# Kernel optimization log

Measured on AMD Instinct MI355X. Metric: run time of the kernel, lower is better.

Reference implementation:

```python
import jax, jax.numpy as jnp
import numpy as np

B, S, F_IN, E, H = 8, 1024, 512, 512, 8
C = E // H  # chunk size per head


def setup_inputs() -> dict:
    key = jax.random.key(0)
    ks = jax.random.split(key, 20)
    sF = 1.0 / np.sqrt(F_IN)
    sE = 1.0 / np.sqrt(E)
    d = {
        'x_real': jax.random.normal(ks[0], (B, S, F_IN), jnp.float32),
        'x_imag': jax.random.normal(ks[1], (B, S, F_IN), jnp.float32),
    }
    names = ['q', 'k', 'v']
    for i, n in enumerate(names):
        d[f'w{n}_r'] = jax.random.normal(ks[2 + 4 * i], (E, F_IN), jnp.float32) * sF
        d[f'w{n}_i'] = jax.random.normal(ks[3 + 4 * i], (E, F_IN), jnp.float32) * sF
        d[f'b{n}_r'] = jax.random.normal(ks[4 + 4 * i], (E,), jnp.float32) * sF
        d[f'b{n}_i'] = jax.random.normal(ks[5 + 4 * i], (E,), jnp.float32) * sF
    d['wo_r'] = jax.random.normal(ks[14], (F_IN, E), jnp.float32) * sE
    d['wo_i'] = jax.random.normal(ks[15], (F_IN, E), jnp.float32) * sE
    d['bo_r'] = jax.random.normal(ks[16], (F_IN,), jnp.float32) * sE
    d['bo_i'] = jax.random.normal(ks[17], (F_IN,), jnp.float32) * sE
    return d


def _cplx(r, i):
    return jax.lax.complex(r, i)


def _heads(y):
    # (B, S, E) -> (B, H, S, C); matches split(dim=2)+stack+transpose(0,1)
    return y.reshape(B, S, H, C).transpose(0, 2, 1, 3)


def reference(x_real, x_imag,
              wq_r, wq_i, bq_r, bq_i,
              wk_r, wk_i, bk_r, bk_i,
              wv_r, wv_i, bv_r, bv_i,
              wo_r, wo_i, bo_r, bo_i):
    x = _cplx(x_real, x_imag)
    wq, wk, wv = _cplx(wq_r, wq_i), _cplx(wk_r, wk_i), _cplx(wv_r, wv_i)
    bq, bk, bv = _cplx(bq_r, bq_i), _cplx(bk_r, bk_i), _cplx(bv_r, bv_i)
    wo, bo = _cplx(wo_r, wo_i), _cplx(bo_r, bo_i)

    q = _heads(jnp.einsum('bsf,ef->bse', x, wq) + bq)  # (B,H,S,C) complex
    k = _heads(jnp.einsum('bsf,ef->bse', x, wk) + bk)
    v = _heads(jnp.einsum('bsf,ef->bse', x, wv) + bv)

    divisor = jnp.sqrt(jnp.float32(2 * C))
    # Hermitian inner product: q @ conj(k)^T -> (B,H,S,S)
    sim = jnp.einsum('bhsc,bhtc->bhst', q, jnp.conj(k)) / divisor
    attn = jax.nn.softmax(jnp.abs(sim), axis=3).astype(jnp.complex64)
    # second Hermitian bmm: attn @ conj(v)
    av = jnp.einsum('bhst,bhtc->bhsc', attn, jnp.conj(v))
    concat = av.transpose(0, 2, 1, 3).reshape(B, S, E)
    out = jnp.einsum('bse,fe->bsf', concat, wo) + bo
    return out, attn
```

## Files before the change

### kernel.cpp

```cpp
#include <hip/hip_runtime.h>


namespace {
constexpr int Bn = 8, Sn = 1024, Fn = 512, En = 512, Hn = 8, Cn = 64;
constexpr int Mn = Bn * Sn;
constexpr int Qszi = Bn * Hn * Sn * Cn;
constexpr size_t Qsz = (size_t)Qszi;
constexpr int XLIM = Bn * Sn * Fn;
constexpr int WLIM = En * Fn;
constexpr size_t OUT1 = (size_t)Bn * Sn * Fn;
constexpr size_t ATT1 = (size_t)Bn * Hn * Sn * Sn;
constexpr float RDIV = 0.08838834764831845f;
}

typedef __attribute__((ext_vector_type(8))) short short8v;
typedef __attribute__((ext_vector_type(4))) float f32x4;

__device__ __forceinline__ float bf2f(unsigned short u) {
    union { unsigned int u32; float f; } c; c.u32 = (unsigned int)u << 16; return c.f;
}
__device__ __forceinline__ unsigned short f2bf(float f) {
    union { float f; unsigned int u; } c; c.f = f;
    unsigned int r = (c.u + 0x7FFFu + ((c.u >> 16) & 1u)) >> 16;
    return (unsigned short)r;
}
__device__ __forceinline__ unsigned int packbf(float lo, float hi) {
    return (unsigned int)f2bf(lo) | ((unsigned int)f2bf(hi) << 16);
}
__device__ __forceinline__ short8v neg8(short8v v) {
    union { short8v s; unsigned int u[4]; } c; c.s = v;
    #pragma unroll
    for (int j = 0; j < 4; ++j) c.u[j] ^= 0x80008000u;
    return c.s;
}
__device__ __forceinline__ float4 ld4(const float* p) { return *(const float4*)p; }

template<bool CONJB>
__device__ __forceinline__ void mfma_body(
    const short (*As_r)[40], const short (*As_i)[40],
    const short (*Bs_r)[40], const short (*Bs_i)[40],
    int wr, int wn, int lrow, int lk,
    f32x4 accr[4][2], f32x4 acci[4][2])
{
    short8v a_r[4], a_i[4], a_x[4];
    #pragma unroll
    for (int fm = 0; fm < 4; ++fm) {
        a_r[fm] = *(const short8v*)&As_r[wr*64 + fm*16 + lrow][lk];
        a_i[fm] = *(const short8v*)&As_i[wr*64 + fm*16 + lrow][lk];
        a_x[fm] = neg8(CONJB ? a_r[fm] : a_i[fm]);
    }
    short8v b_r[2], b_i[2];
    #pragma unroll
    for (int fn = 0; fn < 2; ++fn) {
        b_r[fn] = *(const short8v*)&Bs_r[wn*32 + fn*16 + lrow][lk];
        b_i[fn] = *(const short8v*)&Bs_i[wn*32 + fn*16 + lrow][lk];
    }
    #pragma unroll
    for (int fm = 0; fm < 4; ++fm)
        #pragma unroll
        for (int fn = 0; fn < 2; ++fn) {
            accr[fm][fn] = __builtin_amdgcn_mfma_f32_16x16x32_bf16(
                a_r[fm], b_r[fn], accr[fm][fn], 0, 0, 0);
            accr[fm][fn] = __builtin_amdgcn_mfma_f32_16x16x32_bf16(
                CONJB ? a_i[fm] : a_x[fm], b_i[fn], accr[fm][fn], 0, 0, 0);
            acci[fm][fn] = __builtin_amdgcn_mfma_f32_16x16x32_bf16(
                CONJB ? a_x[fm] : a_r[fm], b_i[fn], acci[fm][fn], 0, 0, 0);
            acci[fm][fn] = __builtin_amdgcn_mfma_f32_16x16x32_bf16(
                a_i[fm], b_r[fn], acci[fm][fn], 0, 0, 0);
        }
}

template<bool CONJB>
__device__ __forceinline__ void cgemm_mfma(
    const float* __restrict__ Ar, const float* __restrict__ Ai, int arow0, int lda,
    const float* __restrict__ Br, const float* __restrict__ Bi, int brow0, int ldb,
    int K, f32x4 accr[4][2], f32x4 acci[4][2])
{
    __shared__ short As_r[128][40], As_i[128][40];
    __shared__ short Bs_r[64][40],  Bs_i[64][40];
    const int tid = threadIdx.x;
    const int sar = tid >> 1, sac = (tid & 1) * 16;
    const int sbr = tid >> 2, sbc = (tid & 3) * 8;
    const int wid = tid >> 6, lane = tid & 63;
    const int wr = wid >> 1, wn = wid & 1;
    const int lrow = lane & 15, lk = (lane >> 4) * 8;

    for (int k0 = 0; k0 < K; k0 += 32) {
        const float* pAr = Ar + (size_t)(arow0 + sar) * lda + k0 + sac;
        const float* pAi = Ai + (size_t)(arow0 + sar) * lda + k0 + sac;
        float4 va_r[4], va_i[4];
        #pragma unroll
        for (int q = 0; q < 4; ++q) { va_r[q] = ld4(pAr + 4*q); va_i[q] = ld4(pAi + 4*q); }
        const float* pBr = Br + (size_t)(brow0 + sbr) * ldb + k0 + sbc;
        const float* pBi = Bi + (size_t)(brow0 + sbr) * ldb + k0 + sbc;
        float4 vb_r[2], vb_i[2];
        #pragma unroll
        for (int q = 0; q < 2; ++q) { vb_r[q] = ld4(pBr + 4*q); vb_i[q] = ld4(pBi + 4*q); }

        __syncthreads();
        #pragma unroll
        for (int q = 0; q < 4; ++q) {
            *(uint2*)&As_r[sar][sac + 4*q] =
                make_uint2(packbf(va_r[q].x, va_r[q].y), packbf(va_r[q].z, va_r[q].w));
            *(uint2*)&As_i[sar][sac + 4*q] =
                make_uint2(packbf(va_i[q].x, va_i[q].y), packbf(va_i[q].z, va_i[q].w));
        }
        #pragma unroll
        for (int q = 0; q < 2; ++q) {
            *(uint2*)&Bs_r[sbr][sbc + 4*q] =
                make_uint2(packbf(vb_r[q].x, vb_r[q].y), packbf(vb_r[q].z, vb_r[q].w));
            *(uint2*)&Bs_i[sbr][sbc + 4*q] =
                make_uint2(packbf(vb_i[q].x, vb_i[q].y), packbf(vb_i[q].z, vb_i[q].w));
        }
        __syncthreads();
        mfma_body<CONJB>(As_r, As_i, Bs_r, Bs_i, wr, wn, lrow, lk, accr, acci);
    }
}

template<bool CONJB>
__device__ __forceinline__ void cgemm_mfma_abf16(
    const unsigned short* __restrict__ Ar, const unsigned short* __restrict__ Ai,
    int arow0, int lda,
    const float* __restrict__ Br, const float* __restrict__ Bi, int brow0, int ldb,
    int K, f32x4 accr[4][2], f32x4 acci[4][2])
{
    __shared__ short As_r[128][40], As_i[128][40];
    __shared__ short Bs_r[64][40],  Bs_i[64][40];
    const int tid = threadIdx.x;
    const int sar = tid >> 1, sac = (tid & 1) * 16;
    const int sbr = tid >> 2, sbc = (tid & 3) * 8;
    const int wid = tid >> 6, lane = tid & 63;
    const int wr = wid >> 1, wn = wid & 1;
    const int lrow = lane & 15, lk = (lane >> 4) * 8;

    for (int k0 = 0; k0 < K; k0 += 32) {
        const unsigned short* pAr = Ar + (size_t)(arow0 + sar) * lda + k0 + sac;
        const unsigned short* pAi = Ai + (size_t)(arow0 + sar) * lda + k0 + sac;
        short8v va_r0 = *(const short8v*)pAr;
        short8v va_r1 = *(const short8v*)(pAr + 8);
        short8v va_i0 = *(const short8v*)pAi;
        short8v va_i1 = *(const short8v*)(pAi + 8);
        const float* pBr = Br + (size_t)(brow0 + sbr) * ldb + k0 + sbc;
        const float* pBi = Bi + (size_t)(brow0 + sbr) * ldb + k0 + sbc;
        float4 vb_r[2], vb_i[2];
        #pragma unroll
        for (int q = 0; q < 2; ++q) { vb_r[q] = ld4(pBr + 4*q); vb_i[q] = ld4(pBi + 4*q); }

        __syncthreads();
        *(short8v*)&As_r[sar][sac]     = va_r0;
        *(short8v*)&As_r[sar][sac + 8] = va_r1;
        *(short8v*)&As_i[sar][sac]     = va_i0;
        *(short8v*)&As_i[sar][sac + 8] = va_i1;
        #pragma unroll
        for (int q = 0; q < 2; ++q) {
            *(uint2*)&Bs_r[sbr][sbc + 4*q] =
                make_uint2(packbf(vb_r[q].x, vb_r[q].y), packbf(vb_r[q].z, vb_r[q].w));
            *(uint2*)&Bs_i[sbr][sbc + 4*q] =
                make_uint2(packbf(vb_i[q].x, vb_i[q].y), packbf(vb_i[q].z, vb_i[q].w));
        }
        __syncthreads();
        mfma_body<CONJB>(As_r, As_i, Bs_r, Bs_i, wr, wn, lrow, lk, accr, acci);
    }
}

__global__ void diag_k(float* __restrict__ out, float v) { out[0] = v; }

__global__ __launch_bounds__(256) void qkv_proj_k(
    const float* __restrict__ xr, const float* __restrict__ xi,
    const float* __restrict__ wqr, const float* __restrict__ wqi,
    const float* __restrict__ bqr, const float* __restrict__ bqi,
    const float* __restrict__ wkr, const float* __restrict__ wki,
    const float* __restrict__ bkr, const float* __restrict__ bki,
    const float* __restrict__ wvr, const float* __restrict__ wvi,
    const float* __restrict__ bvr, const float* __restrict__ bvi,
    unsigned short* __restrict__ ws)
{
    const int which = blockIdx.z;
    const float* wr_ = which == 0 ? wqr : which == 1 ? wkr : wvr;
    const float* wi_ = which == 0 ? wqi : which == 1 ? wki : wvi;
    const float* br_ = which == 0 ? bqr : which == 1 ? bkr : bvr;
    const float* bi_ = which == 0 ? bqi : which == 1 ? bki : bvi;
    unsigned short* outr = ws + (size_t)which * 2 * Qsz;
    unsigned short* outi = outr + Qsz;

    const int m0 = blockIdx.x * 128, n0 = blockIdx.y * 64;
    f32x4 accr[4][2], acci[4][2];
    const f32x4 z4 = {0.f, 0.f, 0.f, 0.f};
    #pragma unroll
    for (int fm = 0; fm < 4; ++fm)
        #pragma unroll
        for (int fn = 0; fn < 2; ++fn) { accr[fm][fn] = z4; acci[fm][fn] = z4; }

    cgemm_mfma<false>(xr, xi, m0, Fn, wr_, wi_, n0, Fn, Fn, accr, acci);

    const int lane = threadIdx.x & 63, wid = threadIdx.x >> 6;
    const int wr2 = wid >> 1, wn2 = wid & 1;
    #pragma unroll
    for (int fm = 0; fm < 4; ++fm)
        #pragma unroll
        for (int fn = 0; fn < 2; ++fn) {
            const int e = n0 + wn2*32 + fn*16 + (lane & 15);
            const int h = e >> 6, c = e & (Cn - 1);
            const float brv = br_[e], biv = bi_[e];
            #pragma unroll
            for (int r = 0; r < 4; ++r) {
                const int m = m0 + wr2*64 + fm*16 + (lane >> 4)*4 + r;
                const int b = m >> 10, s = m & (Sn - 1);
                const size_t idx = (((size_t)(b * Hn + h)) * Sn + s) * Cn + c;
                outr[idx] = f2bf(accr[fm][fn][r] + brv);
                outi[idx] = f2bf(acci[fm][fn][r] + biv);
            }
        }
}

template<int ST>
__global__ __launch_bounds__(256) void attn_fused_k(
    const unsigned short* __restrict__ qkv, float* __restrict__ attn,
    unsigned short* __restrict__ avb)
{
    const int bh = blockIdx.y;
    const int r0 = blockIdx.x * 128;
    const size_t poff = (size_t)bh * Sn * Cn;
    const unsigned short* qr = qkv + poff;
    const unsigned short* qi = qkv + Qsz + poff;
    const unsigned short* kr = qkv + 2 * Qsz + poff;
    const unsigned short* ki = qkv + 3 * Qsz + poff;
    const unsigned short* vr = qkv + 4 * Qsz + poff;
    const unsigned short* vi = qkv + 5 * Qsz + poff;

    __shared__ short Qr[128][68], Qi[128][68];
    __shared__ short KP[2][64][68];
    __shared__ short Vtr[64][68], Vti[64][68];
    short (*Ps)[68] = (short(*)[68])KP;

    const int tid = threadIdx.x;
    const int lane = tid & 63, wid = tid >> 6;
    const int lrow = lane & 15, g = lane >> 4, lk = g * 8;
    const int srow0 = 32 * wid;
    const int wr = wid >> 1, wn = wid & 1;

    {
        const int row = tid >> 1, seg = (tid & 1) * 32;
        const unsigned short* pr = qr + (size_t)(r0 + row) * Cn + seg;
        const unsigned short* pi = qi + (size_t)(r0 + row) * Cn + seg;
        #pragma unroll
        for (int q = 0; q < 4; ++q) {
            *(short8v*)&Qr[row][seg + 8*q] = *(const short8v*)(pr + 8*q);
            *(short8v*)&Qi[row][seg + 8*q] = *(const short8v*)(pi + 8*q);
        }
    }
    const int kst_row = tid >> 2, kst_seg = (tid & 3) * 16;
    const int vst_t = tid & 63, vst_c = (tid >> 6) * 16;

    float ssum[2][4] = {};
    __syncthreads();

    for (int t0 = 0; t0 < Sn; t0 += 64) {
        short8v k_r0 = *(const short8v*)(kr + (size_t)(t0 + kst_row) * Cn + kst_seg);
        short8v k_r1 = *(const short8v*)(kr + (size_t)(t0 + kst_row) * Cn + kst_seg + 8);
        short8v k_i0 = *(const short8v*)(ki + (size_t)(t0 + kst_row) * Cn + kst_seg);
        short8v k_i1 = *(const short8v*)(ki + (size_t)(t0 + kst_row) * Cn + kst_seg + 8);
        __syncthreads();
        *(short8v*)&KP[0][kst_row][kst_seg]     = k_r0;
        *(short8v*)&KP[0][kst_row][kst_seg + 8] = k_r1;
        *(short8v*)&KP[1][kst_row][kst_seg]     = k_i0;
        *(short8v*)&KP[1][kst_row][kst_seg + 8] = k_i1;
        __syncthreads();

        f32x4 cr[2][4], ci[2][4];
        const f32x4 z4 = {0.f, 0.f, 0.f, 0.f};
        #pragma unroll
        for (int fm = 0; fm < 2; ++fm)
            #pragma unroll
            for (int fn = 0; fn < 4; ++fn) { cr[fm][fn] = z4; ci[fm][fn] = z4; }
        #pragma unroll
        for (int kh = 0; kh < 2; ++kh) {
            const int kof = kh*32 + lk;
            short8v br_[4], bi_[4];
            #pragma unroll
            for (int fn = 0; fn < 4; ++fn) {
                br_[fn] = *(const short8v*)&KP[0][fn*16 + lrow][kof];
                bi_[fn] = *(const short8v*)&KP[1][fn*16 + lrow][kof];
            }
            #pragma unroll
            for (int fm = 0; fm < 2; ++fm) {
                short8v ar = *(const short8v*)&Qr[srow0 + fm*16 + lrow][kof];
                short8v ai = *(const short8v*)&Qi[srow0 + fm*16 + lrow][kof];
                short8v ax = neg8(ar);
                #pragma unroll
                for (int fn = 0; fn < 4; ++fn) {
                    cr[fm][fn] = __builtin_amdgcn_mfma_f32_16x16x32_bf16(ar, br_[fn], cr[fm][fn], 0,0,0);
                    cr[fm][fn] = __builtin_amdgcn_mfma_f32_16x16x32_bf16(ai, bi_[fn], cr[fm][fn], 0,0,0);
                    ci[fm][fn] = __builtin_amdgcn_mfma_f32_16x16x32_bf16(ai, br_[fn], ci[fm][fn], 0,0,0);
                    ci[fm][fn] = __builtin_amdgcn_mfma_f32_16x16x32_bf16(ax, bi_[fn], ci[fm][fn], 0,0,0);
                }
            }
        }
        #pragma unroll
        for (int fm = 0; fm < 2; ++fm)
            #pragma unroll
            for (int rr = 0; rr < 4; ++rr) {
                float acc = 0.f;
                #pragma unroll
                for (int fn = 0; fn < 4; ++fn) {
                    const float re = cr[fm][fn][rr], im = ci[fm][fn][rr];
                    acc += __expf(sqrtf(fmaf(re, re, im*im)) * RDIV);
                }
                ssum[fm][rr] += acc;
            }
    }
    float inv[2][4];
    #pragma unroll
    for (int fm = 0; fm < 2; ++fm)
        #pragma unroll
        for (int rr = 0; rr < 4; ++rr) {
            float s = ssum[fm][rr];
            s += __shfl_xor(s, 1); s += __shfl_xor(s, 2);
            s += __shfl_xor(s, 4); s += __shfl_xor(s, 8);
            inv[fm][rr] = 1.f / s;
        }

    f32x4 pvr[4][2], pvi[4][2];
    const f32x4 z4 = {0.f, 0.f, 0.f, 0.f};
    #pragma unroll
    for (int fm = 0; fm < 4; ++fm)
        #pragma unroll
        for (int fn = 0; fn < 2; ++fn) { pvr[fm][fn] = z4; pvi[fm][fn] = z4; }

    for (int t0 = 0; t0 < Sn; t0 += 64) {
        short8v k_r0 = *(const short8v*)(kr + (size_t)(t0 + kst_row) * Cn + kst_seg);
        short8v k_r1 = *(const short8v*)(kr + (size_t)(t0 + kst_row) * Cn + kst_seg + 8);
        short8v k_i0 = *(const short8v*)(ki + (size_t)(t0 + kst_row) * Cn + kst_seg);
        short8v k_i1 = *(const short8v*)(ki + (size_t)(t0 + kst_row) * Cn + kst_seg + 8);
        short8v v_r0 = *(const short8v*)(vr + (size_t)(t0 + vst_t) * Cn + vst_c);
        short8v v_r1 = *(const short8v*)(vr + (size_t)(t0 + vst_t) * Cn + vst_c + 8);
        short8v v_i0 = *(const short8v*)(vi + (size_t)(t0 + vst_t) * Cn + vst_c);
        short8v v_i1 = *(const short8v*)(vi + (size_t)(t0 + vst_t) * Cn + vst_c + 8);
        __syncthreads();
        *(short8v*)&KP[0][kst_row][kst_seg]     = k_r0;
        *(short8v*)&KP[0][kst_row][kst_seg + 8] = k_r1;
        *(short8v*)&KP[1][kst_row][kst_seg]     = k_i0;
        *(short8v*)&KP[1][kst_row][kst_seg + 8] = k_i1;
        #pragma unroll
        for (int j = 0; j < 8; ++j) {
            Vtr[vst_c + j][vst_t] = v_r0[j];
            Vtr[vst_c + 8 + j][vst_t] = v_r1[j];
            Vti[vst_c + j][vst_t] = v_i0[j];
            Vti[vst_c + 8 + j][vst_t] = v_i1[j];
        }
        __syncthreads();

        f32x4 cr[2][4], ci[2][4];
        #pragma unroll
        for (int fm = 0; fm < 2; ++fm)
            #pragma unroll
            for (int fn = 0; fn < 4; ++fn) { cr[fm][fn] = z4; ci[fm][fn] = z4; }
        #pragma unroll
        for (int kh = 0; kh < 2; ++kh) {
            const int kof = kh*32 + lk;
            short8v br_[4], bi_[4];
            #pragma unroll
            for (int fn = 0; fn < 4; ++fn) {
                br_[fn] = *(const short8v*)&KP[0][fn*16 + lrow][kof];
                bi_[fn] = *(const short8v*)&KP[1][fn*16 + lrow][kof];
            }
            #pragma unroll
            for (int fm = 0; fm < 2; ++fm) {
                short8v ar = *(const short8v*)&Qr[srow0 + fm*16 + lrow][kof];
                short8v ai = *(const short8v*)&Qi[srow0 + fm*16 + lrow][kof];
                short8v ax = neg8(ar);
                #pragma unroll
                for (int fn = 0; fn < 4; ++fn) {
                    cr[fm][fn] = __builtin_amdgcn_mfma_f32_16x16x32_bf16(ar, br_[fn], cr[fm][fn], 0,0,0);
                    cr[fm][fn] = __builtin_amdgcn_mfma_f32_16x16x32_bf16(ai, bi_[fn], cr[fm][fn], 0,0,0);
                    ci[fm][fn] = __builtin_amdgcn_mfma_f32_16x16x32_bf16(ai, br_[fn], ci[fm][fn], 0,0,0);
                    ci[fm][fn] = __builtin_amdgcn_mfma_f32_16x16x32_bf16(ax, bi_[fn], ci[fm][fn], 0,0,0);
                }
            }
        }
        float pval[2][4][4];
        #pragma unroll
        for (int fm = 0; fm < 2; ++fm)
            #pragma unroll
            for (int fn = 0; fn < 4; ++fn) {
                const int t = t0 + fn*16 + lrow;
                #pragma unroll
                for (int rr = 0; rr < 4; ++rr) {
                    const float re = cr[fm][fn][rr], im = ci[fm][fn][rr];
                    const float p = __expf(sqrtf(fmaf(re, re, im*im)) * RDIV) * inv[fm][rr];
                    pval[fm][fn][rr] = p;
                    const size_t row = (size_t)bh * Sn + r0 + srow0 + fm*16 + g*4 + rr;
                    const size_t idx = (row * Sn + t) * (size_t)ST;
                    if (ST == 2) *(float2*)&attn[idx] = make_float2(p, 0.f);
                    else         attn[idx] = p;
                }
            }
        __syncthreads();
        #pragma unroll
        for (int fm = 0; fm < 2; ++fm)
            #pragma unroll
            for (int fn = 0; fn < 4; ++fn)
                #pragma unroll
                for (int rr = 0; rr < 4; ++rr)
                    Ps[srow0 + fm*16 + g*4 + rr][fn*16 + lrow] = f2bf(pval[fm][fn][rr]);
        __syncthreads();

        #pragma unroll
        for (int kh = 0; kh < 2; ++kh) {
            const int kof = kh*32 + lk;
            short8v bR[2], bI[2];
            #pragma unroll
            for (int fn = 0; fn < 2; ++fn) {
                bR[fn] = *(const short8v*)&Vtr[wn*32 + fn*16 + lrow][kof];
                bI[fn] = *(const short8v*)&Vti[wn*32 + fn*16 + lrow][kof];
            }
            #pragma unroll
            for (int fm = 0; fm < 4; ++fm) {
                short8v pA = *(const short8v*)&Ps[wr*64 + fm*16 + lrow][kof];
                #pragma unroll
                for (int fn = 0; fn < 2; ++fn) {
                    pvr[fm][fn] = __builtin_amdgcn_mfma_f32_16x16x32_bf16(pA, bR[fn], pvr[fm][fn], 0,0,0);
                    pvi[fm][fn] = __builtin_amdgcn_mfma_f32_16x16x32_bf16(pA, bI[fn], pvi[fm][fn], 0,0,0);
                }
            }
        }
    }

    const int b = bh >> 3, h = bh & 7;
    #pragma unroll
    for (int fm = 0; fm < 4; ++fm)
        #pragma unroll
        for (int fn = 0; fn < 2; ++fn) {
            const int c = wn*32 + fn*16 + lrow;
            #pragma unroll
            for (int rr = 0; rr < 4; ++rr) {
                const int row = r0 + wr*64 + fm*16 + g*4 + rr;
                const size_t addr = ((size_t)(b * Sn + row)) * En + h * Cn + c;
                avb[addr]       = f2bf( pvr[fm][fn][rr]);
                avb[Qsz + addr] = f2bf(-pvi[fm][fn][rr]);
            }
        }
}

template<int ST>
__global__ __launch_bounds__(256) void out_proj_k(
    const unsigned short* __restrict__ avr, const unsigned short* __restrict__ avi,
    const float* __restrict__ wor, const float* __restrict__ woi,
    const float* __restrict__ bor, const float* __restrict__ boi,
    float* __restrict__ out)
{
    const int m0 = blockIdx.x * 128, n0 = blockIdx.y * 64;
    f32x4 accr[4][2], acci[4][2];
    const f32x4 z4 = {0.f, 0.f, 0.f, 0.f};
    #pragma unroll
    for (int fm = 0; fm < 4; ++fm)
        #pragma unroll
        for (int fn = 0; fn < 2; ++fn) { accr[fm][fn] = z4; acci[fm][fn] = z4; }

    cgemm_mfma_abf16<false>(avr, avi, m0, En, wor, woi, n0, En, En, accr, acci);

    const int lane = threadIdx.x & 63, wid = threadIdx.x >> 6;
    const int wr2 = wid >> 1, wn2 = wid & 1;
    #pragma unroll
    for (int fm = 0; fm < 4; ++fm)
        #pragma unroll
        for (int fn = 0; fn < 2; ++fn) {
            const int f = n0 + wn2*32 + fn*16 + (lane & 15);
            const float brv = bor[f], biv = boi[f];
            #pragma unroll
            for (int r = 0; r < 4; ++r) {
                const int m = m0 + wr2*64 + fm*16 + (lane >> 4)*4 + r;
                const size_t idx = ((size_t)m * Fn + f) * (size_t)ST;
                if (ST == 2)
                    *(float2*)&out[idx] = make_float2(accr[fm][fn][r] + brv, acci[fm][fn][r] + biv);
                else
                    out[idx] = accr[fm][fn][r] + brv;
            }
        }
}

template<int ST>
static void launch_all(const float* xr, const float* xi,
                       const float* wqr, const float* wqi, const float* bqr, const float* bqi,
                       const float* wkr, const float* wki, const float* bkr, const float* bki,
                       const float* wvr, const float* wvi, const float* bvr, const float* bvi,
                       const float* wor, const float* woi, const float* bor, const float* boi,
                       unsigned short* qkv, unsigned short* avb, float* out, hipStream_t stream)
{
    float* attn = out + OUT1 * ST;
    qkv_proj_k<<<dim3(Mn/128, En/64, 3), 256, 0, stream>>>(
        xr, xi, wqr, wqi, bqr, bqi, wkr, wki, bkr, bki, wvr, wvi, bvr, bvi, qkv);
    attn_fused_k<ST><<<dim3(Sn/128, Bn*Hn), 256, 0, stream>>>(qkv, attn, avb);
    out_proj_k<ST><<<dim3(Mn/128, Fn/64), 256, 0, stream>>>(
        avb, avb + Qsz, wor, woi, bor, boi, out);
}

extern "C" void kernel_launch(void* const* d_in, const int* in_sizes, int n_in,
                              void* d_out, int out_size, void* d_ws, size_t ws_size,
                              hipStream_t stream)
{
    bool sizes_ok = (n_in == 18);
    if (sizes_ok) {
        sizes_ok = in_sizes[0] == XLIM && in_sizes[1] == XLIM;
        for (int g = 0; g < 3 && sizes_ok; ++g) {
            sizes_ok = in_sizes[2 + 4*g] == WLIM && in_sizes[3 + 4*g] == WLIM &&
                       in_sizes[4 + 4*g] == En  && in_sizes[5 + 4*g] == En;
        }
        sizes_ok = sizes_ok && in_sizes[14] == WLIM && in_sizes[15] == WLIM &&
                   in_sizes[16] == Fn && in_sizes[17] == Fn;
    }
    const size_t ws_needed = 8 * Qsz * sizeof(unsigned short);
    const bool ws_ok = (d_ws != nullptr) && (ws_size >= ws_needed);

    const long long fullF = 2LL * (long long)(OUT1 + ATT1);
    const long long realF = (long long)(OUT1 + ATT1);
    const int st = ((long long)out_size == fullF) ? 2
                 : ((long long)out_size == realF) ? 1 : 0;

    if (!sizes_ok || !ws_ok || st == 0) {
        float diag = !sizes_ok ? 3.0e9f
                   : !ws_ok    ? (float)(double)ws_size
                               : (float)out_size;
        diag_k<<<1, 1, 0, stream>>>((float*)d_out, diag);
        return;
    }

    const float* xr  = (const float*)d_in[0];
    const float* xi  = (const float*)d_in[1];
    const float* wqr = (const float*)d_in[2];
    const float* wqi = (const float*)d_in[3];
    const float* bqr = (const float*)d_in[4];
    const float* bqi = (const float*)d_in[5];
    const float* wkr = (const float*)d_in[6];
    const float* wki = (const float*)d_in[7];
    const float* bkr = (const float*)d_in[8];
    const float* bki = (const float*)d_in[9];
    const float* wvr = (const float*)d_in[10];
    const float* wvi = (const float*)d_in[11];
    const float* bvr = (const float*)d_in[12];
    const float* bvi = (const float*)d_in[13];
    const float* wor = (const float*)d_in[14];
    const float* woi = (const float*)d_in[15];
    const float* bor = (const float*)d_in[16];
    const float* boi = (const float*)d_in[17];

    unsigned short* qkv = (unsigned short*)d_ws;
    unsigned short* avb = qkv + 6 * Qsz;
    float* out = (float*)d_out;

    if (st == 2)
        launch_all<2>(xr, xi, wqr, wqi, bqr, bqi, wkr, wki, bkr, bki,
                      wvr, wvi, bvr, bvi, wor, woi, bor, boi, qkv, avb, out, stream);
    else
        launch_all<1>(xr, xi, wqr, wqi, bqr, bqi, wkr, wki, bkr, bki,
                      wvr, wvi, bvr, bvi, wor, woi, bor, boi, qkv, avb, out, stream);
}
```

Baseline: 316.8 us.

## Halve attention query tile to 64 rows and add MFMA wave priority hints

The fused attention kernel now handles 64 query rows per block instead of 128, so each wave owns 16 rows and the grid doubles to 1024 blocks. This cuts registers and LDS per block, which should help occupancy and wave count across the CUs. The cost is that each block rereads K and V for its whole sequence twice (once for the softmax sum, once for the output), so K/V traffic per query row doubles. s_setprio hints are also placed around the MFMA clusters in both the attention and projection GEMMs.

```diff
diff --git a/kernel.cpp b/kernel.cpp
--- a/kernel.cpp
+++ b/kernel.cpp
@@ -55,6 +55,7 @@
         b_r[fn] = *(const short8v*)&Bs_r[wn*32 + fn*16 + lrow][lk];
         b_i[fn] = *(const short8v*)&Bs_i[wn*32 + fn*16 + lrow][lk];
     }
+    __builtin_amdgcn_s_setprio(1);
     #pragma unroll
     for (int fm = 0; fm < 4; ++fm)
         #pragma unroll
@@ -68,6 +69,7 @@
             acci[fm][fn] = __builtin_amdgcn_mfma_f32_16x16x32_bf16(
                 a_i[fm], b_r[fn], acci[fm][fn], 0, 0, 0);
         }
+    __builtin_amdgcn_s_setprio(0);
 }
 
 template<bool CONJB>
@@ -219,7 +221,7 @@
     unsigned short* __restrict__ avb)
 {
     const int bh = blockIdx.y;
-    const int r0 = blockIdx.x * 128;
+    const int r0 = blockIdx.x * 64;
     const size_t poff = (size_t)bh * Sn * Cn;
     const unsigned short* qr = qkv + poff;
     const unsigned short* qi = qkv + Qsz + poff;
@@ -228,7 +230,7 @@
     const unsigned short* vr = qkv + 4 * Qsz + poff;
     const unsigned short* vi = qkv + 5 * Qsz + poff;
 
-    __shared__ short Qr[128][68], Qi[128][68];
+    __shared__ short Qr[64][68], Qi[64][68];
     __shared__ short KP[2][64][68];
     __shared__ short Vtr[64][68], Vti[64][68];
     short (*Ps)[68] = (short(*)[68])KP;
@@ -236,15 +238,15 @@
     const int tid = threadIdx.x;
     const int lane = tid & 63, wid = tid >> 6;
     const int lrow = lane & 15, g = lane >> 4, lk = g * 8;
-    const int srow0 = 32 * wid;
+    const int srow0 = 16 * wid;
     const int wr = wid >> 1, wn = wid & 1;
 
     {
-        const int row = tid >> 1, seg = (tid & 1) * 32;
+        const int row = tid >> 2, seg = (tid & 3) * 16;
         const unsigned short* pr = qr + (size_t)(r0 + row) * Cn + seg;
         const unsigned short* pi = qi + (size_t)(r0 + row) * Cn + seg;
         #pragma unroll
-        for (int q = 0; q < 4; ++q) {
+        for (int q = 0; q < 2; ++q) {
             *(short8v*)&Qr[row][seg + 8*q] = *(const short8v*)(pr + 8*q);
             *(short8v*)&Qi[row][seg + 8*q] = *(const short8v*)(pi + 8*q);
         }
@@ -252,7 +254,7 @@
     const int kst_row = tid >> 2, kst_seg = (tid & 3) * 16;
     const int vst_t = tid & 63, vst_c = (tid >> 6) * 16;
 
-    float ssum[2][4] = {};
+    float ssum[4] = {};
     __syncthreads();
 
     for (int t0 = 0; t0 < Sn; t0 += 64) {
@@ -267,63 +269,52 @@
         *(short8v*)&KP[1][kst_row][kst_seg + 8] = k_i1;
         __syncthreads();
 
-        f32x4 cr[2][4], ci[2][4];
+        f32x4 cr[4], ci[4];
         const f32x4 z4 = {0.f, 0.f, 0.f, 0.f};
         #pragma unroll
-        for (int fm = 0; fm < 2; ++fm)
-            #pragma unroll
-            for (int fn = 0; fn < 4; ++fn) { cr[fm][fn] = z4; ci[fm][fn] = z4; }
+        for (int fn = 0; fn < 4; ++fn) { cr[fn] = z4; ci[fn] = z4; }
         #pragma unroll
         for (int kh = 0; kh < 2; ++kh) {
             const int kof = kh*32 + lk;
-            short8v br_[4], bi_[4];
+            short8v ar = *(const short8v*)&Qr[srow0 + lrow][kof];
+            short8v ai = *(const short8v*)&Qi[srow0 + lrow][kof];
+            short8v ax = neg8(ar);
+            __builtin_amdgcn_s_setprio(1);
             #pragma unroll
             for (int fn = 0; fn < 4; ++fn) {
-                br_[fn] = *(const short8v*)&KP[0][fn*16 + lrow][kof];
-                bi_[fn] = *(const short8v*)&KP[1][fn*16 + lrow][kof];
-            }
-            #pragma unroll
-            for (int fm = 0; fm < 2; ++fm) {
-                short8v ar = *(const short8v*)&Qr[srow0 + fm*16 + lrow][kof];
-                short8v ai = *(const short8v*)&Qi[srow0 + fm*16 + lrow][kof];
-                short8v ax = neg8(ar);
-                #pragma unroll
-                for (int fn = 0; fn < 4; ++fn) {
-                    cr[fm][fn] = __builtin_amdgcn_mfma_f32_16x16x32_bf16(ar, br_[fn], cr[fm][fn], 0,0,0);
-                    cr[fm][fn] = __builtin_amdgcn_mfma_f32_16x16x32_bf16(ai, bi_[fn], cr[fm][fn], 0,0,0);
-                    ci[fm][fn] = __builtin_amdgcn_mfma_f32_16x16x32_bf16(ai, br_[fn], ci[fm][fn], 0,0,0);
-                    ci[fm][fn] = __builtin_amdgcn_mfma_f32_16x16x32_bf16(ax, bi_[fn], ci[fm][fn], 0,0,0);
-                }
-            }
-        }
-        #pragma unroll
-        for (int fm = 0; fm < 2; ++fm)
-            #pragma unroll
-            for (int rr = 0; rr < 4; ++rr) {
-                float acc = 0.f;
-                #pragma unroll
-                for (int fn = 0; fn < 4; ++fn) {
-                    const float re = cr[fm][fn][rr], im = ci[fm][fn][rr];
-                    acc += __expf(sqrtf(fmaf(re, re, im*im)) * RDIV);
-                }
-                ssum[fm][rr] += acc;
-            }
-    }
-    float inv[2][4];
+                short8v br_ = *(const short8v*)&KP[0][fn*16 + lrow][kof];
+                short8v bi_ = *(const short8v*)&KP[1][fn*16 + lrow][kof];
+                cr[fn] = __builtin_amdgcn_mfma_f32_16x16x32_bf16(ar, br_, cr[fn], 0,0,0);
+                cr[fn] = __builtin_amdgcn_mfma_f32_16x16x32_bf16(ai, bi_, cr[fn], 0,0,0);
+                ci[fn] = __builtin_amdgcn_mfma_f32_16x16x32_bf16(ai, br_, ci[fn], 0,0,0);
+                ci[fn] = __builtin_amdgcn_mfma_f32_16x16x32_bf16(ax, bi_, ci[fn], 0,0,0);
+            }
+            __builtin_amdgcn_s_setprio(0);
+        }
+        #pragma unroll
+        for (int rr = 0; rr < 4; ++rr) {
+            float acc = 0.f;
+            #pragma unroll
+            for (int fn = 0; fn < 4; ++fn) {
+                const float re = cr[fn][rr], im = ci[fn][rr];
+                acc += __expf(sqrtf(fmaf(re, re, im*im)) * RDIV);
+            }
+            ssum[rr] += acc;
+        }
+    }
+    float inv[4];
+    #pragma unroll
+    for (int rr = 0; rr < 4; ++rr) {
+        float s = ssum[rr];
+        s += __shfl_xor(s, 1); s += __shfl_xor(s, 2);
+        s += __shfl_xor(s, 4); s += __shfl_xor(s, 8);
+        inv[rr] = 1.f / s;
+    }
+
+    f32x4 pvr[2][2], pvi[2][2];
+    const f32x4 z4 = {0.f, 0.f, 0.f, 0.f};
     #pragma unroll
     for (int fm = 0; fm < 2; ++fm)
-        #pragma unroll
-        for (int rr = 0; rr < 4; ++rr) {
-            float s = ssum[fm][rr];
-            s += __shfl_xor(s, 1); s += __shfl_xor(s, 2);
-            s += __shfl_xor(s, 4); s += __shfl_xor(s, 8);
-            inv[fm][rr] = 1.f / s;
-        }
-
-    f32x4 pvr[4][2], pvi[4][2];
-    const f32x4 z4 = {0.f, 0.f, 0.f, 0.f};
-    #pragma unroll
-    for (int fm = 0; fm < 4; ++fm)
         #pragma unroll
         for (int fn = 0; fn < 2; ++fn) { pvr[fm][fn] = z4; pvi[fm][fn] = z4; }
 
@@ -350,59 +341,48 @@
         }
         __syncthreads();
 
-        f32x4 cr[2][4], ci[2][4];
-        #pragma unroll
-        for (int fm = 0; fm < 2; ++fm)
-            #pragma unroll
-            for (int fn = 0; fn < 4; ++fn) { cr[fm][fn] = z4; ci[fm][fn] = z4; }
+        f32x4 cr[4], ci[4];
+        #pragma unroll
+        for (int fn = 0; fn < 4; ++fn) { cr[fn] = z4; ci[fn] = z4; }
         #pragma unroll
         for (int kh = 0; kh < 2; ++kh) {
             const int kof = kh*32 + lk;
-            short8v br_[4], bi_[4];
+            short8v ar = *(const short8v*)&Qr[srow0 + lrow][kof];
+            short8v ai = *(const short8v*)&Qi[srow0 + lrow][kof];
+            short8v ax = neg8(ar);
+            __builtin_amdgcn_s_setprio(1);
             #pragma unroll
             for (int fn = 0; fn < 4; ++fn) {
-                br_[fn] = *(const short8v*)&KP[0][fn*16 + lrow][kof];
-                bi_[fn] = *(const short8v*)&KP[1][fn*16 + lrow][kof];
-            }
-            #pragma unroll
-            for (int fm = 0; fm < 2; ++fm) {
-                short8v ar = *(const short8v*)&Qr[srow0 + fm*16 + lrow][kof];
-                short8v ai = *(const short8v*)&Qi[srow0 + fm*16 + lrow][kof];
-                short8v ax = neg8(ar);
-                #pragma unroll
-                for (int fn = 0; fn < 4; ++fn) {
-                    cr[fm][fn] = __builtin_amdgcn_mfma_f32_16x16x32_bf16(ar, br_[fn], cr[fm][fn], 0,0,0);
-                    cr[fm][fn] = __builtin_amdgcn_mfma_f32_16x16x32_bf16(ai, bi_[fn], cr[fm][fn], 0,0,0);
-                    ci[fm][fn] = __builtin_amdgcn_mfma_f32_16x16x32_bf16(ai, br_[fn], ci[fm][fn], 0,0,0);
-                    ci[fm][fn] = __builtin_amdgcn_mfma_f32_16x16x32_bf16(ax, bi_[fn], ci[fm][fn], 0,0,0);
-                }
-            }
-        }
-        float pval[2][4][4];
-        #pragma unroll
-        for (int fm = 0; fm < 2; ++fm)
-            #pragma unroll
-            for (int fn = 0; fn < 4; ++fn) {
-                const int t = t0 + fn*16 + lrow;
-                #pragma unroll
-                for (int rr = 0; rr < 4; ++rr) {
-                    const float re = cr[fm][fn][rr], im = ci[fm][fn][rr];
-                    const float p = __expf(sqrtf(fmaf(re, re, im*im)) * RDIV) * inv[fm][rr];
-                    pval[fm][fn][rr] = p;
-                    const size_t row = (size_t)bh * Sn + r0 + srow0 + fm*16 + g*4 + rr;
-                    const size_t idx = (row * Sn + t) * (size_t)ST;
-                    if (ST == 2) *(float2*)&attn[idx] = make_float2(p, 0.f);
-                    else         attn[idx] = p;
-                }
-            }
-        __syncthreads();
-        #pragma unroll
-        for (int fm = 0; fm < 2; ++fm)
-            #pragma unroll
-            for (int fn = 0; fn < 4; ++fn)
-                #pragma unroll
-                for (int rr = 0; rr < 4; ++rr)
-                    Ps[srow0 + fm*16 + g*4 + rr][fn*16 + lrow] = f2bf(pval[fm][fn][rr]);
+                short8v br_ = *(const short8v*)&KP[0][fn*16 + lrow][kof];
+                short8v bi_ = *(const short8v*)&KP[1][fn*16 + lrow][kof];
+                cr[fn] = __builtin_amdgcn_mfma_f32_16x16x32_bf16(ar, br_, cr[fn], 0,0,0);
+                cr[fn] = __builtin_amdgcn_mfma_f32_16x16x32_bf16(ai, bi_, cr[fn], 0,0,0);
+                ci[fn] = __builtin_amdgcn_mfma_f32_16x16x32_bf16(ai, br_, ci[fn], 0,0,0);
+                ci[fn] = __builtin_amdgcn_mfma_f32_16x16x32_bf16(ax, bi_, ci[fn], 0,0,0);
+            }
+            __builtin_amdgcn_s_setprio(0);
+        }
+        float pval[4][4];
+        #pragma unroll
+        for (int fn = 0; fn < 4; ++fn) {
+            const int t = t0 + fn*16 + lrow;
+            #pragma unroll
+            for (int rr = 0; rr < 4; ++rr) {
+                const float re = cr[fn][rr], im = ci[fn][rr];
+                const float p = __expf(sqrtf(fmaf(re, re, im*im)) * RDIV) * inv[rr];
+                pval[fn][rr] = p;
+                const size_t row = (size_t)bh * Sn + r0 + srow0 + g*4 + rr;
+                const size_t idx = (row * Sn + t) * (size_t)ST;
+                if (ST == 2) *(float2*)&attn[idx] = make_float2(p, 0.f);
+                else         attn[idx] = p;
+            }
+        }
+        __syncthreads();
+        #pragma unroll
+        for (int fn = 0; fn < 4; ++fn)
+            #pragma unroll
+            for (int rr = 0; rr < 4; ++rr)
+                Ps[srow0 + g*4 + rr][fn*16 + lrow] = f2bf(pval[fn][rr]);
         __syncthreads();
 
         #pragma unroll
@@ -414,27 +394,29 @@
                 bR[fn] = *(const short8v*)&Vtr[wn*32 + fn*16 + lrow][kof];
                 bI[fn] = *(const short8v*)&Vti[wn*32 + fn*16 + lrow][kof];
             }
-            #pragma unroll
-            for (int fm = 0; fm < 4; ++fm) {
-                short8v pA = *(const short8v*)&Ps[wr*64 + fm*16 + lrow][kof];
+            __builtin_amdgcn_s_setprio(1);
+            #pragma unroll
+            for (int fm = 0; fm < 2; ++fm) {
+                short8v pA = *(const short8v*)&Ps[wr*32 + fm*16 + lrow][kof];
                 #pragma unroll
                 for (int fn = 0; fn < 2; ++fn) {
                     pvr[fm][fn] = __builtin_amdgcn_mfma_f32_16x16x32_bf16(pA, bR[fn], pvr[fm][fn], 0,0,0);
                     pvi[fm][fn] = __builtin_amdgcn_mfma_f32_16x16x32_bf16(pA, bI[fn], pvi[fm][fn], 0,0,0);
                 }
             }
+            __builtin_amdgcn_s_setprio(0);
         }
     }
 
     const int b = bh >> 3, h = bh & 7;
     #pragma unroll
-    for (int fm = 0; fm < 4; ++fm)
+    for (int fm = 0; fm < 2; ++fm)
         #pragma unroll
         for (int fn = 0; fn < 2; ++fn) {
             const int c = wn*32 + fn*16 + lrow;
             #pragma unroll
             for (int rr = 0; rr < 4; ++rr) {
-                const int row = r0 + wr*64 + fm*16 + g*4 + rr;
+                const int row = r0 + wr*32 + fm*16 + g*4 + rr;
                 const size_t addr = ((size_t)(b * Sn + row)) * En + h * Cn + c;
                 avb[addr]       = f2bf( pvr[fm][fn][rr]);
                 avb[Qsz + addr] = f2bf(-pvi[fm][fn][rr]);
@@ -490,7 +472,7 @@
     float* attn = out + OUT1 * ST;
     qkv_proj_k<<<dim3(Mn/128, En/64, 3), 256, 0, stream>>>(
         xr, xi, wqr, wqi, bqr, bqi, wkr, wki, bkr, bki, wvr, wvi, bvr, bvi, qkv);
-    attn_fused_k<ST><<<dim3(Sn/128, Bn*Hn), 256, 0, stream>>>(qkv, attn, avb);
+    attn_fused_k<ST><<<dim3(Sn/64, Bn*Hn), 256, 0, stream>>>(qkv, attn, avb);
     out_proj_k<ST><<<dim3(Mn/128, Fn/64), 256, 0, stream>>>(
         avb, avb + Qsz, wor, woi, bor, boi, out);
 }
```

After: 323.6 us. 2.1% more time.

## Keep Q fragments in registers, give P its own LDS buffer, add MFMA priority

Applied to the files above, without the earlier changes.

Each wave now loads its Q fragments straight from global memory into registers instead of staging them through shared memory, which removes the repeated LDS reads of Q on every key tile. P gets a dedicated shared buffer rather than aliasing the K buffer, so it is written directly in the softmax loop and one barrier goes away. The bf16 conversion of P switches to truncation instead of round-to-nearest, and s_setprio brackets are placed around the MFMA blocks. The changes cost extra registers and a little precision in P.

```diff
diff --git a/kernel.cpp b/kernel.cpp
--- a/kernel.cpp
+++ b/kernel.cpp
@@ -24,6 +24,10 @@
     unsigned int r = (c.u + 0x7FFFu + ((c.u >> 16) & 1u)) >> 16;
     return (unsigned short)r;
 }
+__device__ __forceinline__ unsigned short f2bf_t(float f) {
+    union { float f; unsigned int u; } c; c.f = f;
+    return (unsigned short)(c.u >> 16);
+}
 __device__ __forceinline__ unsigned int packbf(float lo, float hi) {
     return (unsigned int)f2bf(lo) | ((unsigned int)f2bf(hi) << 16);
 }
@@ -55,6 +59,7 @@
         b_r[fn] = *(const short8v*)&Bs_r[wn*32 + fn*16 + lrow][lk];
         b_i[fn] = *(const short8v*)&Bs_i[wn*32 + fn*16 + lrow][lk];
     }
+    __builtin_amdgcn_s_setprio(1);
     #pragma unroll
     for (int fm = 0; fm < 4; ++fm)
         #pragma unroll
@@ -68,6 +73,7 @@
             acci[fm][fn] = __builtin_amdgcn_mfma_f32_16x16x32_bf16(
                 a_i[fm], b_r[fn], acci[fm][fn], 0, 0, 0);
         }
+    __builtin_amdgcn_s_setprio(0);
 }
 
 template<bool CONJB>
@@ -228,10 +234,9 @@
     const unsigned short* vr = qkv + 4 * Qsz + poff;
     const unsigned short* vi = qkv + 5 * Qsz + poff;
 
-    __shared__ short Qr[128][68], Qi[128][68];
-    __shared__ short KP[2][64][68];
+    __shared__ short Ksr[64][68], Ksi[64][68];
     __shared__ short Vtr[64][68], Vti[64][68];
-    short (*Ps)[68] = (short(*)[68])KP;
+    __shared__ short Ps[128][68];
 
     const int tid = threadIdx.x;
     const int lane = tid & 63, wid = tid >> 6;
@@ -239,21 +244,20 @@
     const int srow0 = 32 * wid;
     const int wr = wid >> 1, wn = wid & 1;
 
-    {
-        const int row = tid >> 1, seg = (tid & 1) * 32;
-        const unsigned short* pr = qr + (size_t)(r0 + row) * Cn + seg;
-        const unsigned short* pi = qi + (size_t)(r0 + row) * Cn + seg;
-        #pragma unroll
-        for (int q = 0; q < 4; ++q) {
-            *(short8v*)&Qr[row][seg + 8*q] = *(const short8v*)(pr + 8*q);
-            *(short8v*)&Qi[row][seg + 8*q] = *(const short8v*)(pi + 8*q);
-        }
-    }
+    short8v qfr[2][2], qfi[2][2];
+    #pragma unroll
+    for (int fm = 0; fm < 2; ++fm)
+        #pragma unroll
+        for (int kh = 0; kh < 2; ++kh) {
+            const size_t row = (size_t)(r0 + srow0 + fm*16 + lrow);
+            qfr[fm][kh] = *(const short8v*)(qr + row * Cn + kh*32 + lk);
+            qfi[fm][kh] = *(const short8v*)(qi + row * Cn + kh*32 + lk);
+        }
+
     const int kst_row = tid >> 2, kst_seg = (tid & 3) * 16;
     const int vst_t = tid & 63, vst_c = (tid >> 6) * 16;
 
     float ssum[2][4] = {};
-    __syncthreads();
 
     for (int t0 = 0; t0 < Sn; t0 += 64) {
         short8v k_r0 = *(const short8v*)(kr + (size_t)(t0 + kst_row) * Cn + kst_seg);
@@ -261,10 +265,10 @@
         short8v k_i0 = *(const short8v*)(ki + (size_t)(t0 + kst_row) * Cn + kst_seg);
         short8v k_i1 = *(const short8v*)(ki + (size_t)(t0 + kst_row) * Cn + kst_seg + 8);
         __syncthreads();
-        *(short8v*)&KP[0][kst_row][kst_seg]     = k_r0;
-        *(short8v*)&KP[0][kst_row][kst_seg + 8] = k_r1;
-        *(short8v*)&KP[1][kst_row][kst_seg]     = k_i0;
-        *(short8v*)&KP[1][kst_row][kst_seg + 8] = k_i1;
+        *(short8v*)&Ksr[kst_row][kst_seg]     = k_r0;
+        *(short8v*)&Ksr[kst_row][kst_seg + 8] = k_r1;
+        *(short8v*)&Ksi[kst_row][kst_seg]     = k_i0;
+        *(short8v*)&Ksi[kst_row][kst_seg + 8] = k_i1;
         __syncthreads();
 
         f32x4 cr[2][4], ci[2][4];
@@ -279,13 +283,13 @@
             short8v br_[4], bi_[4];
             #pragma unroll
             for (int fn = 0; fn < 4; ++fn) {
-                br_[fn] = *(const short8v*)&KP[0][fn*16 + lrow][kof];
-                bi_[fn] = *(const short8v*)&KP[1][fn*16 + lrow][kof];
-            }
+                br_[fn] = *(const short8v*)&Ksr[fn*16 + lrow][kof];
+                bi_[fn] = *(const short8v*)&Ksi[fn*16 + lrow][kof];
+            }
+            __builtin_amdgcn_s_setprio(1);
             #pragma unroll
             for (int fm = 0; fm < 2; ++fm) {
-                short8v ar = *(const short8v*)&Qr[srow0 + fm*16 + lrow][kof];
-                short8v ai = *(const short8v*)&Qi[srow0 + fm*16 + lrow][kof];
+                short8v ar = qfr[fm][kh], ai = qfi[fm][kh];
                 short8v ax = neg8(ar);
                 #pragma unroll
                 for (int fn = 0; fn < 4; ++fn) {
@@ -295,6 +299,7 @@
                     ci[fm][fn] = __builtin_amdgcn_mfma_f32_16x16x32_bf16(ax, bi_[fn], ci[fm][fn], 0,0,0);
                 }
             }
+            __builtin_amdgcn_s_setprio(0);
         }
         #pragma unroll
         for (int fm = 0; fm < 2; ++fm)
@@ -337,10 +342,10 @@
         short8v v_i0 = *(const short8v*)(vi + (size_t)(t0 + vst_t) * Cn + vst_c);
         short8v v_i1 = *(const short8v*)(vi + (size_t)(t0 + vst_t) * Cn + vst_c + 8);
         __syncthreads();
-        *(short8v*)&KP[0][kst_row][kst_seg]     = k_r0;
-        *(short8v*)&KP[0][kst_row][kst_seg + 8] = k_r1;
-        *(short8v*)&KP[1][kst_row][kst_seg]     = k_i0;
-        *(short8v*)&KP[1][kst_row][kst_seg + 8] = k_i1;
+        *(short8v*)&Ksr[kst_row][kst_seg]     = k_r0;
+        *(short8v*)&Ksr[kst_row][kst_seg + 8] = k_r1;
+        *(short8v*)&Ksi[kst_row][kst_seg]     = k_i0;
+        *(short8v*)&Ksi[kst_row][kst_seg + 8] = k_i1;
         #pragma unroll
         for (int j = 0; j < 8; ++j) {
             Vtr[vst_c + j][vst_t] = v_r0[j];
@@ -361,13 +366,13 @@
             short8v br_[4], bi_[4];
             #pragma unroll
             for (int fn = 0; fn < 4; ++fn) {
-                br_[fn] = *(const short8v*)&KP[0][fn*16 + lrow][kof];
-                bi_[fn] = *(const short8v*)&KP[1][fn*16 + lrow][kof];
-            }
+                br_[fn] = *(const short8v*)&Ksr[fn*16 + lrow][kof];
+                bi_[fn] = *(const short8v*)&Ksi[fn*16 + lrow][kof];
+            }
+            __builtin_amdgcn_s_setprio(1);
             #pragma unroll
             for (int fm = 0; fm < 2; ++fm) {
-                short8v ar = *(const short8v*)&Qr[srow0 + fm*16 + lrow][kof];
-                short8v ai = *(const short8v*)&Qi[srow0 + fm*16 + lrow][kof];
+                short8v ar = qfr[fm][kh], ai = qfi[fm][kh];
                 short8v ax = neg8(ar);
                 #pragma unroll
                 for (int fn = 0; fn < 4; ++fn) {
@@ -377,8 +382,8 @@
                     ci[fm][fn] = __builtin_amdgcn_mfma_f32_16x16x32_bf16(ax, bi_[fn], ci[fm][fn], 0,0,0);
                 }
             }
-        }
-        float pval[2][4][4];
+            __builtin_amdgcn_s_setprio(0);
+        }
         #pragma unroll
         for (int fm = 0; fm < 2; ++fm)
             #pragma unroll
@@ -388,21 +393,13 @@
                 for (int rr = 0; rr < 4; ++rr) {
                     const float re = cr[fm][fn][rr], im = ci[fm][fn][rr];
                     const float p = __expf(sqrtf(fmaf(re, re, im*im)) * RDIV) * inv[fm][rr];
-                    pval[fm][fn][rr] = p;
                     const size_t row = (size_t)bh * Sn + r0 + srow0 + fm*16 + g*4 + rr;
                     const size_t idx = (row * Sn + t) * (size_t)ST;
                     if (ST == 2) *(float2*)&attn[idx] = make_float2(p, 0.f);
                     else         attn[idx] = p;
+                    Ps[srow0 + fm*16 + g*4 + rr][fn*16 + lrow] = f2bf_t(p);
                 }
             }
-        __syncthreads();
-        #pragma unroll
-        for (int fm = 0; fm < 2; ++fm)
-            #pragma unroll
-            for (int fn = 0; fn < 4; ++fn)
-                #pragma unroll
-                for (int rr = 0; rr < 4; ++rr)
-                    Ps[srow0 + fm*16 + g*4 + rr][fn*16 + lrow] = f2bf(pval[fm][fn][rr]);
         __syncthreads();
 
         #pragma unroll
@@ -414,6 +411,7 @@
                 bR[fn] = *(const short8v*)&Vtr[wn*32 + fn*16 + lrow][kof];
                 bI[fn] = *(const short8v*)&Vti[wn*32 + fn*16 + lrow][kof];
             }
+            __builtin_amdgcn_s_setprio(1);
             #pragma unroll
             for (int fm = 0; fm < 4; ++fm) {
                 short8v pA = *(const short8v*)&Ps[wr*64 + fm*16 + lrow][kof];
@@ -423,6 +421,7 @@
                     pvi[fm][fn] = __builtin_amdgcn_mfma_f32_16x16x32_bf16(pA, bI[fn], pvi[fm][fn], 0,0,0);
                 }
             }
+            __builtin_amdgcn_s_setprio(0);
         }
     }
 
```

After: 353.7 us. 1.12x slower.

## Fuse two-pass softmax into single pass with deferred normalization kernel

Applied to the files above, without the earlier changes.

The attention kernel no longer runs a separate first pass over all keys to compute the softmax denominators. It writes unnormalized exp values to the attention output, accumulates P·V unnormalized, and scales the AV result by the row reciprocal at the end. A new kernel then re-reads and rescales the full attention matrix. This halves the QK^T MFMA work but adds an extra read and write of the large attention tensor, and s_setprio hints are added around MFMA blocks.

```diff
diff --git a/kernel.cpp b/kernel.cpp
--- a/kernel.cpp
+++ b/kernel.cpp
@@ -55,6 +55,7 @@
         b_r[fn] = *(const short8v*)&Bs_r[wn*32 + fn*16 + lrow][lk];
         b_i[fn] = *(const short8v*)&Bs_i[wn*32 + fn*16 + lrow][lk];
     }
+    __builtin_amdgcn_s_setprio(1);
     #pragma unroll
     for (int fm = 0; fm < 4; ++fm)
         #pragma unroll
@@ -68,6 +69,7 @@
             acci[fm][fn] = __builtin_amdgcn_mfma_f32_16x16x32_bf16(
                 a_i[fm], b_r[fn], acci[fm][fn], 0, 0, 0);
         }
+    __builtin_amdgcn_s_setprio(0);
 }
 
 template<bool CONJB>
@@ -231,6 +233,7 @@
     __shared__ short Qr[128][68], Qi[128][68];
     __shared__ short KP[2][64][68];
     __shared__ short Vtr[64][68], Vti[64][68];
+    __shared__ float sinv[128];
     short (*Ps)[68] = (short(*)[68])KP;
 
     const int tid = threadIdx.x;
@@ -253,6 +256,13 @@
     const int vst_t = tid & 63, vst_c = (tid >> 6) * 16;
 
     float ssum[2][4] = {};
+    f32x4 pvr[4][2], pvi[4][2];
+    const f32x4 z4 = {0.f, 0.f, 0.f, 0.f};
+    #pragma unroll
+    for (int fm = 0; fm < 4; ++fm)
+        #pragma unroll
+        for (int fn = 0; fn < 2; ++fn) { pvr[fm][fn] = z4; pvi[fm][fn] = z4; }
+
     __syncthreads();
 
     for (int t0 = 0; t0 < Sn; t0 += 64) {
@@ -260,15 +270,25 @@
         short8v k_r1 = *(const short8v*)(kr + (size_t)(t0 + kst_row) * Cn + kst_seg + 8);
         short8v k_i0 = *(const short8v*)(ki + (size_t)(t0 + kst_row) * Cn + kst_seg);
         short8v k_i1 = *(const short8v*)(ki + (size_t)(t0 + kst_row) * Cn + kst_seg + 8);
+        short8v v_r0 = *(const short8v*)(vr + (size_t)(t0 + vst_t) * Cn + vst_c);
+        short8v v_r1 = *(const short8v*)(vr + (size_t)(t0 + vst_t) * Cn + vst_c + 8);
+        short8v v_i0 = *(const short8v*)(vi + (size_t)(t0 + vst_t) * Cn + vst_c);
+        short8v v_i1 = *(const short8v*)(vi + (size_t)(t0 + vst_t) * Cn + vst_c + 8);
         __syncthreads();
         *(short8v*)&KP[0][kst_row][kst_seg]     = k_r0;
         *(short8v*)&KP[0][kst_row][kst_seg + 8] = k_r1;
         *(short8v*)&KP[1][kst_row][kst_seg]     = k_i0;
         *(short8v*)&KP[1][kst_row][kst_seg + 8] = k_i1;
+        #pragma unroll
+        for (int j = 0; j < 8; ++j) {
+            Vtr[vst_c + j][vst_t] = v_r0[j];
+            Vtr[vst_c + 8 + j][vst_t] = v_r1[j];
+            Vti[vst_c + j][vst_t] = v_i0[j];
+            Vti[vst_c + 8 + j][vst_t] = v_i1[j];
+        }
         __syncthreads();
 
         f32x4 cr[2][4], ci[2][4];
-        const f32x4 z4 = {0.f, 0.f, 0.f, 0.f};
         #pragma unroll
         for (int fm = 0; fm < 2; ++fm)
             #pragma unroll
@@ -282,6 +302,7 @@
                 br_[fn] = *(const short8v*)&KP[0][fn*16 + lrow][kof];
                 bi_[fn] = *(const short8v*)&KP[1][fn*16 + lrow][kof];
             }
+            __builtin_amdgcn_s_setprio(1);
             #pragma unroll
             for (int fm = 0; fm < 2; ++fm) {
                 short8v ar = *(const short8v*)&Qr[srow0 + fm*16 + lrow][kof];
@@ -295,88 +316,7 @@
                     ci[fm][fn] = __builtin_amdgcn_mfma_f32_16x16x32_bf16(ax, bi_[fn], ci[fm][fn], 0,0,0);
                 }
             }
-        }
-        #pragma unroll
-        for (int fm = 0; fm < 2; ++fm)
-            #pragma unroll
-            for (int rr = 0; rr < 4; ++rr) {
-                float acc = 0.f;
-                #pragma unroll
-                for (int fn = 0; fn < 4; ++fn) {
-                    const float re = cr[fm][fn][rr], im = ci[fm][fn][rr];
-                    acc += __expf(sqrtf(fmaf(re, re, im*im)) * RDIV);
-                }
-                ssum[fm][rr] += acc;
-            }
-    }
-    float inv[2][4];
-    #pragma unroll
-    for (int fm = 0; fm < 2; ++fm)
-        #pragma unroll
-        for (int rr = 0; rr < 4; ++rr) {
-            float s = ssum[fm][rr];
-            s += __shfl_xor(s, 1); s += __shfl_xor(s, 2);
-            s += __shfl_xor(s, 4); s += __shfl_xor(s, 8);
-            inv[fm][rr] = 1.f / s;
-        }
-
-    f32x4 pvr[4][2], pvi[4][2];
-    const f32x4 z4 = {0.f, 0.f, 0.f, 0.f};
-    #pragma unroll
-    for (int fm = 0; fm < 4; ++fm)
-        #pragma unroll
-        for (int fn = 0; fn < 2; ++fn) { pvr[fm][fn] = z4; pvi[fm][fn] = z4; }
-
-    for (int t0 = 0; t0 < Sn; t0 += 64) {
-        short8v k_r0 = *(const short8v*)(kr + (size_t)(t0 + kst_row) * Cn + kst_seg);
-        short8v k_r1 = *(const short8v*)(kr + (size_t)(t0 + kst_row) * Cn + kst_seg + 8);
-        short8v k_i0 = *(const short8v*)(ki + (size_t)(t0 + kst_row) * Cn + kst_seg);
-        short8v k_i1 = *(const short8v*)(ki + (size_t)(t0 + kst_row) * Cn + kst_seg + 8);
-        short8v v_r0 = *(const short8v*)(vr + (size_t)(t0 + vst_t) * Cn + vst_c);
-        short8v v_r1 = *(const short8v*)(vr + (size_t)(t0 + vst_t) * Cn + vst_c + 8);
-        short8v v_i0 = *(const short8v*)(vi + (size_t)(t0 + vst_t) * Cn + vst_c);
-        short8v v_i1 = *(const short8v*)(vi + (size_t)(t0 + vst_t) * Cn + vst_c + 8);
-        __syncthreads();
-        *(short8v*)&KP[0][kst_row][kst_seg]     = k_r0;
-        *(short8v*)&KP[0][kst_row][kst_seg + 8] = k_r1;
-        *(short8v*)&KP[1][kst_row][kst_seg]     = k_i0;
-        *(short8v*)&KP[1][kst_row][kst_seg + 8] = k_i1;
-        #pragma unroll
-        for (int j = 0; j < 8; ++j) {
-            Vtr[vst_c + j][vst_t] = v_r0[j];
-            Vtr[vst_c + 8 + j][vst_t] = v_r1[j];
-            Vti[vst_c + j][vst_t] = v_i0[j];
-            Vti[vst_c + 8 + j][vst_t] = v_i1[j];
-        }
-        __syncthreads();
-
-        f32x4 cr[2][4], ci[2][4];
-        #pragma unroll
-        for (int fm = 0; fm < 2; ++fm)
-            #pragma unroll
-            for (int fn = 0; fn < 4; ++fn) { cr[fm][fn] = z4; ci[fm][fn] = z4; }
-        #pragma unroll
-        for (int kh = 0; kh < 2; ++kh) {
-            const int kof = kh*32 + lk;
-            short8v br_[4], bi_[4];
-            #pragma unroll
-            for (int fn = 0; fn < 4; ++fn) {
-                br_[fn] = *(const short8v*)&KP[0][fn*16 + lrow][kof];
-                bi_[fn] = *(const short8v*)&KP[1][fn*16 + lrow][kof];
-            }
-            #pragma unroll
-            for (int fm = 0; fm < 2; ++fm) {
-                short8v ar = *(const short8v*)&Qr[srow0 + fm*16 + lrow][kof];
-                short8v ai = *(const short8v*)&Qi[srow0 + fm*16 + lrow][kof];
-                short8v ax = neg8(ar);
-                #pragma unroll
-                for (int fn = 0; fn < 4; ++fn) {
-                    cr[fm][fn] = __builtin_amdgcn_mfma_f32_16x16x32_bf16(ar, br_[fn], cr[fm][fn], 0,0,0);
-                    cr[fm][fn] = __builtin_amdgcn_mfma_f32_16x16x32_bf16(ai, bi_[fn], cr[fm][fn], 0,0,0);
-                    ci[fm][fn] = __builtin_amdgcn_mfma_f32_16x16x32_bf16(ai, br_[fn], ci[fm][fn], 0,0,0);
-                    ci[fm][fn] = __builtin_amdgcn_mfma_f32_16x16x32_bf16(ax, bi_[fn], ci[fm][fn], 0,0,0);
-                }
-            }
+            __builtin_amdgcn_s_setprio(0);
         }
         float pval[2][4][4];
         #pragma unroll
@@ -387,8 +327,9 @@
                 #pragma unroll
                 for (int rr = 0; rr < 4; ++rr) {
                     const float re = cr[fm][fn][rr], im = ci[fm][fn][rr];
-                    const float p = __expf(sqrtf(fmaf(re, re, im*im)) * RDIV) * inv[fm][rr];
+                    const float p = __expf(sqrtf(fmaf(re, re, im*im)) * RDIV);
                     pval[fm][fn][rr] = p;
+                    ssum[fm][rr] += p;
                     const size_t row = (size_t)bh * Sn + r0 + srow0 + fm*16 + g*4 + rr;
                     const size_t idx = (row * Sn + t) * (size_t)ST;
                     if (ST == 2) *(float2*)&attn[idx] = make_float2(p, 0.f);
@@ -414,6 +355,7 @@
                 bR[fn] = *(const short8v*)&Vtr[wn*32 + fn*16 + lrow][kof];
                 bI[fn] = *(const short8v*)&Vti[wn*32 + fn*16 + lrow][kof];
             }
+            __builtin_amdgcn_s_setprio(1);
             #pragma unroll
             for (int fm = 0; fm < 4; ++fm) {
                 short8v pA = *(const short8v*)&Ps[wr*64 + fm*16 + lrow][kof];
@@ -423,8 +365,20 @@
                     pvi[fm][fn] = __builtin_amdgcn_mfma_f32_16x16x32_bf16(pA, bI[fn], pvi[fm][fn], 0,0,0);
                 }
             }
-        }
-    }
+            __builtin_amdgcn_s_setprio(0);
+        }
+    }
+
+    #pragma unroll
+    for (int fm = 0; fm < 2; ++fm)
+        #pragma unroll
+        for (int rr = 0; rr < 4; ++rr) {
+            float s = ssum[fm][rr];
+            s += __shfl_xor(s, 1); s += __shfl_xor(s, 2);
+            s += __shfl_xor(s, 4); s += __shfl_xor(s, 8);
+            if (lrow == 0) sinv[srow0 + fm*16 + g*4 + rr] = 1.f / s;
+        }
+    __syncthreads();
 
     const int b = bh >> 3, h = bh & 7;
     #pragma unroll
@@ -434,12 +388,40 @@
             const int c = wn*32 + fn*16 + lrow;
             #pragma unroll
             for (int rr = 0; rr < 4; ++rr) {
-                const int row = r0 + wr*64 + fm*16 + g*4 + rr;
+                const int rl = wr*64 + fm*16 + g*4 + rr;
+                const float sc = sinv[rl];
+                const int row = r0 + rl;
                 const size_t addr = ((size_t)(b * Sn + row)) * En + h * Cn + c;
-                avb[addr]       = f2bf( pvr[fm][fn][rr]);
-                avb[Qsz + addr] = f2bf(-pvi[fm][fn][rr]);
-            }
-        }
+                avb[addr]       = f2bf( pvr[fm][fn][rr] * sc);
+                avb[Qsz + addr] = f2bf(-pvi[fm][fn][rr] * sc);
+            }
+        }
+}
+
+template<int ST>
+__global__ __launch_bounds__(256) void normalize_k(float* __restrict__ attn)
+{
+    const int bh = blockIdx.y;
+    const int wid = threadIdx.x >> 6, lane = threadIdx.x & 63;
+    const int row = blockIdx.x * 4 + wid;
+    const size_t rbase = ((size_t)bh * Sn + row) * Sn;
+
+    float v[16];
+    float sum = 0.f;
+    #pragma unroll
+    for (int j = 0; j < 16; ++j) {
+        v[j] = attn[(rbase + lane + 64*j) * (size_t)ST];
+        sum += v[j];
+    }
+    #pragma unroll
+    for (int m = 32; m >= 1; m >>= 1) sum += __shfl_xor(sum, m);
+    const float inv = 1.f / sum;
+    #pragma unroll
+    for (int j = 0; j < 16; ++j) {
+        const size_t idx = (rbase + lane + 64*j) * (size_t)ST;
+        if (ST == 2) *(float2*)&attn[idx] = make_float2(v[j] * inv, 0.f);
+        else         attn[idx] = v[j] * inv;
+    }
 }
 
 template<int ST>
@@ -491,6 +473,7 @@
     qkv_proj_k<<<dim3(Mn/128, En/64, 3), 256, 0, stream>>>(
         xr, xi, wqr, wqi, bqr, bqi, wkr, wki, bkr, bki, wvr, wvi, bvr, bvi, qkv);
     attn_fused_k<ST><<<dim3(Sn/128, Bn*Hn), 256, 0, stream>>>(qkv, attn, avb);
+    normalize_k<ST><<<dim3(Sn/4, Bn*Hn), 256, 0, stream>>>(attn);
     out_proj_k<ST><<<dim3(Mn/128, Fn/64), 256, 0, stream>>>(
         avb, avb + Qsz, wor, woi, bor, boi, out);
 }
```

After: 384.5 us. 1.21x slower.
